# Optimization experiments

Measured on AMD Instinct MI355X. Metric: run time of the kernel, lower is better.

The kernel has to match this reference:

```python
import jax, jax.numpy as jnp
import numpy as np

B, N, D = 512, 100000, 64
TAU = 1e-4            # gumbel-softmax temperature from source
SIM_RATIO = 0.5       # similarity_ratio init kwarg
COS_EPS = 1e-6


def setup_inputs() -> dict:
    key = jax.random.key(0)
    k1, k2, k3, k4, k5 = jax.random.split(key, 5)
    need_replace = jax.random.randint(k1, (B, 2), 0, N, dtype=jnp.int64) if jax.config.jax_enable_x64 else jax.random.randint(k1, (B, 2), 0, N, dtype=jnp.int32)
    union_feature = jax.random.normal(k2, (B, 2 * D), dtype=jnp.float32)
    all_items = jax.random.normal(k3, (N, D), dtype=jnp.float32) * 0.1
    W = jax.random.normal(k4, (D, 2 * D), dtype=jnp.float32) * 0.05
    b = jax.random.normal(k5, (D,), dtype=jnp.float32) * 0.01
    return {"need_replace": need_replace, "union_feature": union_feature,
            "all_items": all_items, "W": W, "b": b}


def _cosine(a, b):
    # torch.nn.CosineSimilarity(dim=1, eps=1e-6): dot / max(||a||*||b||, eps)
    dot = jnp.sum(a * b, axis=1)
    na = jnp.linalg.norm(a, axis=1)
    nb = jnp.linalg.norm(b, axis=1)
    return dot / jnp.maximum(na * nb, COS_EPS)


def reference(need_replace, union_feature, all_items, W, b):
    item_ids = need_replace[:, 1]
    items_emb = all_items[item_ids]                      # [B, D]
    uif = union_feature @ W.T + b                        # [B, D] (nn.Linear)
    score = uif @ all_items.T                            # [B, N]

    # gumbel_softmax(tau=1e-4, hard=True), training branch
    g = jax.random.gumbel(jax.random.key(42), score.shape, dtype=score.dtype)
    y_soft = jax.nn.softmax((score + g) / TAU, axis=-1)  # [B, N]
    idx = jnp.argmax(y_soft, axis=-1)                    # [B]
    y_hard = jax.nn.one_hot(idx, N, dtype=score.dtype)
    P = y_hard + y_soft - jax.lax.stop_gradient(y_soft)  # straight-through hard one-hot

    item_sequence = jnp.arange(N, dtype=score.dtype)[None, :]
    replaceable_items = jnp.sum(P * item_sequence, axis=-1).astype(jnp.int32)
    replaceable_feat = P @ all_items                     # [B, D]

    sim = _cosine(items_emb, replaceable_feat)
    sim = (sim + 1.0) / 2.0                              # regularize_similarity
    labels = jnp.full((B,), SIM_RATIO, dtype=sim.dtype)
    similarity_loss = jnp.mean((sim - labels) ** 2)      # SimilarityMarginLoss (assumed MSE-to-margin)
    return replaceable_items, replaceable_feat, similarity_loss, jnp.mean(sim)
```

## Files before the change

### kernel.cpp

```cpp
#include <hip/hip_runtime.h>
#include <cstdint>

#define NITEMS   100000
#define BROWS    512
#define DDIM     64
#define S_BLOCKS 391
#define IPB      256
#define NCHUNKS  782
#define FB_Y     8
#define OUT_FEAT 512
#define OUT_LOSS (512 + 512 * 64)
#define OUT_MSIM (OUT_LOSS + 1)

#define BITS_RAW_T 4284334592u
#define G_TE       6.001f

typedef __attribute__((ext_vector_type(8)))  short  bf16x8;
typedef __attribute__((ext_vector_type(16))) float  f32x16;
typedef unsigned long long u64;
typedef uint32_t u32;

#define ROTL(x, r) __builtin_amdgcn_alignbit((x), (x), 32u - (r))

__device__ __forceinline__ u32 threefry_0_42_xor(u32 e) {
    const u32 K1 = 42u;
    const u32 K2 = 0x1BD11BDAu ^ 42u;
    u32 x0 = 0u;
    u32 x1 = e + K1;
#define TFR(r) { x0 += x1; x1 = ROTL(x1, r) ^ x0; }
    TFR(13u) TFR(15u) TFR(26u) TFR(6u)
    x0 += K1;  x1 += K2 + 1u;
    TFR(17u) TFR(29u) TFR(16u) TFR(24u)
    x0 += K2;  x1 += 2u;
    TFR(13u) TFR(15u) TFR(26u) TFR(6u)
    x1 += K1 + 3u;
    TFR(17u) TFR(29u) TFR(16u) TFR(24u)
    x0 += K1;  x1 += K2 + 4u;
    TFR(13u) TFR(15u) TFR(26u) TFR(6u)
    x0 += K2;  x1 += 5u;
#undef TFR
    return x0 ^ x1;
}

__device__ __forceinline__ float gumbel_from_bits(u32 b) {
    float f = __uint_as_float((b >> 9) | 0x3F800000u) - 1.0f;
    f = fmaxf(f, 1.17549435e-38f);
    return -logf(-logf(f));
}
__device__ __forceinline__ u32 order_map(float v) {
    u32 x = __float_as_uint(v);
    return (x & 0x80000000u) ? ~x : (x | 0x80000000u);
}
__device__ __forceinline__ float unpack_val(u64 p) {
    u32 x = (u32)(p >> 32);
    u32 f = (x & 0x80000000u) ? (x & 0x7FFFFFFFu) : ~x;
    return __uint_as_float(f);
}
__device__ __forceinline__ short f32_to_bf16_rne(float f) {
    u32 b = __float_as_uint(f);
    u32 r = (b + 0x7FFFu + ((b >> 16) & 1u)) >> 16;
    return (short)r;
}
__device__ __forceinline__ float bf16_to_f32(short h) {
    return __uint_as_float(((u32)(uint16_t)h) << 16);
}

__global__ void prep_kernel(const float* __restrict__ UF, const float* __restrict__ W,
                            const float* __restrict__ bias, const float* __restrict__ A,
                            float* __restrict__ uif, float* __restrict__ unorm,
                            float* __restrict__ wsAM4, int* __restrict__ cnt,
                            int* __restrict__ done, float* __restrict__ out) {
    const int t = threadIdx.x, b = blockIdx.x;
    if (b == 0) {
        if (t == 0) { *cnt = 0; out[OUT_LOSS] = 0.f; out[OUT_MSIM] = 0.f; }
        done[t] = 0; done[t + 256] = 0;
    }
    if (b < 128) {
        __shared__ float Wt[128 * 65];
        for (int i = t; i < 8192; i += 256) {
            int d = i >> 7, k = i & 127;
            Wt[k * 65 + d] = W[i];
        }
        __syncthreads();
        const int row = b * 4 + (t >> 6);
        const int d   = t & 63;
        const float* u = UF + row * 128;
        float s = 0.f;
#pragma unroll 4
        for (int k = 0; k < 128; k++) s = fmaf(u[k], Wt[k * 65 + d], s);
        s += bias[d];
        uif[row * 64 + d] = s;
        float q = s * s;
#pragma unroll
        for (int o = 32; o >= 1; o >>= 1) q += __shfl_xor(q, o);
        if (d == 0) unorm[row] = sqrtf(q);
    } else {
        const int item = (b - 128) * 256 + t;
        float q = 0.f;
        if (item < NITEMS) {
            const float4* r = (const float4*)(A + (size_t)item * DDIM);
#pragma unroll
            for (int k = 0; k < 16; k++) {
                float4 x = r[k];
                q = fmaf(x.x, x.x, q); q = fmaf(x.y, x.y, q);
                q = fmaf(x.z, x.z, q); q = fmaf(x.w, x.w, q);
            }
        }
        float n = sqrtf(q);
#pragma unroll
        for (int o = 32; o >= 1; o >>= 1) n = fmaxf(n, __shfl_xor(n, o));
        if ((t & 63) == 0) wsAM4[(b - 128) * 4 + (t >> 6)] = n;
    }
}

__global__ __launch_bounds__(256, 4) void phase1_kernel(
        const float* __restrict__ A, const float* __restrict__ uif,
        u64* __restrict__ wsT1, float* __restrict__ wsB) {
    __shared__ bf16x8 sh_ah[4 * 64];
    __shared__ bf16x8 sh_al[4 * 64];
    const int tid  = threadIdx.x;
    const int lane = tid & 63;
    const int wv   = tid >> 6;
    const int rg   = blockIdx.y;
    const int sb   = blockIdx.x;
    const int itembase = sb * IPB;
    const int ntiles = min(8, (NITEMS - itembase + 31) >> 5);
    const int row   = rg * 128 + wv * 32 + (lane & 31);
    const int khalf = (lane >> 5) * 8;

    bf16x8 uh[4], ul[4];
#pragma unroll
    for (int s = 0; s < 4; s++) {
        const float* src = uif + row * 64 + khalf + 16 * s;
        float4 v0 = *(const float4*)src;
        float4 v1 = *(const float4*)(src + 4);
        float vv[8] = {v0.x, v0.y, v0.z, v0.w, v1.x, v1.y, v1.z, v1.w};
        bf16x8 h, l2;
#pragma unroll
        for (int j = 0; j < 8; j++) {
            short hh = f32_to_bf16_rne(vv[j]);
            float r  = vv[j] - bf16_to_f32(hh);
            h[j] = hh; l2[j] = f32_to_bf16_rne(r);
        }
        uh[s] = h; ul[s] = l2;
    }

    u64 t1p = 0ull; float t1f = -3.0e38f, t2f = -3.0e38f, sm = -3.0e38f;
    const u32 rowbase_e = (u32)row * (u32)NITEMS;

    const int s_i   = tid & 31;
    const int s_c   = tid >> 5;
    const int s_dst = (s_c >> 1) * 64 + s_i + 32 * (s_c & 1);
    const float* s_srcbase = A + (size_t)s_i * 64 + 8 * s_c;

    float4 p0 = *(const float4*)(s_srcbase + (size_t)itembase * 64);
    float4 p1 = *(const float4*)(s_srcbase + (size_t)itembase * 64 + 4);

    for (int t = 0; t < ntiles; t++) {
        const int tb = itembase + t * 32;
        bf16x8 h, l2;
        {
            float vv[8] = {p0.x, p0.y, p0.z, p0.w, p1.x, p1.y, p1.z, p1.w};
#pragma unroll
            for (int j = 0; j < 8; j++) {
                short hh = f32_to_bf16_rne(vv[j]);
                float r  = vv[j] - bf16_to_f32(hh);
                h[j] = hh; l2[j] = f32_to_bf16_rne(r);
            }
        }
        __syncthreads();
        sh_ah[s_dst] = h; sh_al[s_dst] = l2;
        __syncthreads();
        if (t + 1 < ntiles) {
            const float* src = s_srcbase + (size_t)(tb + 32) * 64;
            p0 = *(const float4*)src;
            p1 = *(const float4*)(src + 4);
        }

        f32x16 acc;
#pragma unroll
        for (int z = 0; z < 16; z++) acc[z] = 0.0f;
#pragma unroll
        for (int s = 0; s < 4; s++) {
            bf16x8 ah = sh_ah[s * 64 + lane];
            bf16x8 al = sh_al[s * 64 + lane];
            acc = __builtin_amdgcn_mfma_f32_32x32x16_bf16(ah, uh[s], acc, 0, 0, 0);
            acc = __builtin_amdgcn_mfma_f32_32x32x16_bf16(al, uh[s], acc, 0, 0, 0);
            acc = __builtin_amdgcn_mfma_f32_32x32x16_bf16(ah, ul[s], acc, 0, 0, 0);
        }

        const int ib4 = tb + 4 * (lane >> 5);
#pragma unroll
        for (int i = 0; i < 16; i++) {
            const int il   = (i & 3) + 8 * (i >> 2);
            const int item = ib4 + il;
            u32 rb  = threefry_0_42_xor(rowbase_e + (u32)item);
            float s = acc[i];
            sm = fmaxf(sm, s);
            if (rb >= BITS_RAW_T) {
                float g = gumbel_from_bits(rb);
                float v = s + g;
                if (v > t1f) {
                    t2f = t1f; t1f = v;
                    t1p = ((u64)order_map(v) << 32) | (u32)(~(u32)item);
                } else t2f = fmaxf(t2f, v);
            }
        }
    }

    float bnd = fmaxf(t2f, sm + G_TE);
    {
        u64   op = __shfl_xor(t1p, 32);
        float of = __shfl_xor(t1f, 32);
        float ob = __shfl_xor(bnd, 32);
        if (op > t1p) { bnd = fmaxf(fmaxf(bnd, ob), t1f); t1p = op; t1f = of; }
        else          { bnd = fmaxf(fmaxf(bnd, ob), of); }
    }
    if (lane < 32) {
        wsT1[(size_t)row * S_BLOCKS + sb] = t1p;
        wsB [(size_t)row * S_BLOCKS + sb] = bnd;
    }
}

__global__ void merge_kernel(const u64* __restrict__ wsT1, const float* __restrict__ wsB,
                             const float* __restrict__ wsAM4, const float* __restrict__ unorm,
                             const float* __restrict__ A, const int* __restrict__ need_replace,
                             u64* __restrict__ packed, int* __restrict__ rowlist,
                             int* __restrict__ cnt, float* __restrict__ out) {
    const int row = blockIdx.x, t = threadIdx.x;
    float am = 0.f;
    for (int i = t; i < S_BLOCKS * 4; i += 64) am = fmaxf(am, wsAM4[i]);
    u64 p1 = 0ull; float f1 = -3.0e38f, f2 = -3.0e38f;
    for (int sbk = t; sbk < S_BLOCKS; sbk += 64) {
        u64   ep = wsT1[(size_t)row * S_BLOCKS + sbk];
        float e2 = wsB [(size_t)row * S_BLOCKS + sbk];
        if (ep > p1) { f2 = fmaxf(fmaxf(f1, e2), f2); p1 = ep; f1 = unpack_val(ep); }
        else         { float v = unpack_val(ep); f2 = fmaxf(f2, fmaxf(v, e2)); }
    }
#pragma unroll
    for (int off = 1; off < 64; off <<= 1) {
        u64   op  = __shfl_xor(p1, off);
        float of1 = __shfl_xor(f1, off);
        float of2 = __shfl_xor(f2, off);
        am = fmaxf(am, __shfl_xor(am, off));
        if (op > p1) { f2 = fmaxf(fmaxf(f1, of2), f2); p1 = op; f1 = of1; }
        else         { f2 = fmaxf(f2, fmaxf(of1, of2)); }
    }
    const float E = 1.5e-4f * unorm[row] * am + 3.0e-5f;
    if (f1 - f2 > 2.0f * E) {
        const int idx = (int)(~(u32)(p1 & 0xFFFFFFFFull));
        float fr = A[(size_t)idx * DDIM + t];
        out[OUT_FEAT + row * DDIM + t] = fr;
        int   item = need_replace[2 * row + 1];
        float fa   = A[(size_t)item * DDIM + t];
        float dot = fa * fr, na2 = fa * fa, nb2 = fr * fr;
#pragma unroll
        for (int o = 32; o >= 1; o >>= 1) {
            dot += __shfl_down(dot, o);
            na2 += __shfl_down(na2, o);
            nb2 += __shfl_down(nb2, o);
        }
        if (t == 0) {
            out[row] = (float)idx;
            float denom = fmaxf(sqrtf(na2) * sqrtf(nb2), 1e-6f);
            float sim = (dot / denom + 1.0f) * 0.5f;
            float d = sim - 0.5f;
            atomicAdd(&out[OUT_LOSS], d * d * (1.0f / 512.0f));
            atomicAdd(&out[OUT_MSIM], sim * (1.0f / 512.0f));
        }
    } else if (t == 0) {
        packed[row] = 0ull;
        rowlist[atomicAdd(cnt, 1)] = row;
    }
}

__global__ void fallback_kernel(const float* __restrict__ A, const float* __restrict__ uif,
                                const int* __restrict__ rowlist, const int* __restrict__ cnt,
                                const int* __restrict__ need_replace,
                                u64* __restrict__ packed, int* __restrict__ done,
                                float* __restrict__ out) {
    __shared__ float As[128 * 65];
    __shared__ float Us[64];
    __shared__ int   sh_last;
    const int t  = threadIdx.x;
    const int c  = blockIdx.x;
    const int n0 = c * 128;
    const int nitem = min(128, NITEMS - n0);
    const int total = *cnt;
    if ((int)blockIdx.y >= total) return;

    if (t < nitem) {
        const float4* src = (const float4*)(A + (size_t)(n0 + t) * 64);
#pragma unroll
        for (int k4 = 0; k4 < 16; k4++) {
            float4 x = src[k4];
            As[t * 65 + 4 * k4 + 0] = x.x; As[t * 65 + 4 * k4 + 1] = x.y;
            As[t * 65 + 4 * k4 + 2] = x.z; As[t * 65 + 4 * k4 + 3] = x.w;
        }
    }
    for (int li = blockIdx.y; li < total; li += FB_Y) {
        const int row = rowlist[li];
        __syncthreads();
        if (t < 64) Us[t] = uif[row * 64 + t];
        __syncthreads();
        u64 pk = 0ull;
        if (t < nitem) {
            const int item = n0 + t;
            u32 rb  = threefry_0_42_xor((u32)row * (u32)NITEMS + (u32)item);
            float g = gumbel_from_bits(rb);
            float s0 = 0.f, s1 = 0.f;
#pragma unroll
            for (int k8 = 0; k8 < 64; k8 += 8) {
                s0 = fmaf(As[t * 65 + k8 + 0], Us[k8 + 0], s0);
                s0 = fmaf(As[t * 65 + k8 + 1], Us[k8 + 1], s0);
                s0 = fmaf(As[t * 65 + k8 + 2], Us[k8 + 2], s0);
                s0 = fmaf(As[t * 65 + k8 + 3], Us[k8 + 3], s0);
                s1 = fmaf(As[t * 65 + k8 + 4], Us[k8 + 4], s1);
                s1 = fmaf(As[t * 65 + k8 + 5], Us[k8 + 5], s1);
                s1 = fmaf(As[t * 65 + k8 + 6], Us[k8 + 6], s1);
                s1 = fmaf(As[t * 65 + k8 + 7], Us[k8 + 7], s1);
            }
            float v = (s0 + s1) + g;
            pk = ((u64)order_map(v) << 32) | (u32)(~(u32)item);
        }
#pragma unroll
        for (int off = 1; off < 64; off <<= 1) {
            u64 o = __shfl_xor(pk, off);
            pk = (o > pk) ? o : pk;
        }
        if ((t & 63) == 0) atomicMax(&packed[row], pk);
        __syncthreads();
        if (t == 0) {
            __threadfence();
            sh_last = (atomicAdd(&done[li], 1) == NCHUNKS - 1) ? 1 : 0;
        }
        __syncthreads();
        if (sh_last && t < 64) {
            u64 fin = atomicMax(&packed[row], 0ull);
            const int idx = (int)(~(u32)(fin & 0xFFFFFFFFull));
            float fr = A[(size_t)idx * DDIM + t];
            out[OUT_FEAT + row * DDIM + t] = fr;
            int   item = need_replace[2 * row + 1];
            float fa   = A[(size_t)item * DDIM + t];
            float dot = fa * fr, na2 = fa * fa, nb2 = fr * fr;
#pragma unroll
            for (int o = 32; o >= 1; o >>= 1) {
                dot += __shfl_down(dot, o);
                na2 += __shfl_down(na2, o);
                nb2 += __shfl_down(nb2, o);
            }
            if (t == 0) {
                out[row] = (float)idx;
                float denom = fmaxf(sqrtf(na2) * sqrtf(nb2), 1e-6f);
                float sim = (dot / denom + 1.0f) * 0.5f;
                float d = sim - 0.5f;
                atomicAdd(&out[OUT_LOSS], d * d * (1.0f / 512.0f));
                atomicAdd(&out[OUT_MSIM], sim * (1.0f / 512.0f));
            }
        }
        __syncthreads();
    }
}

extern "C" void kernel_launch(void* const* d_in, const int* in_sizes, int n_in,
                              void* d_out, int out_size, void* d_ws, size_t ws_size,
                              hipStream_t stream) {
    (void)in_sizes; (void)n_in; (void)out_size; (void)ws_size;
    const int*   need_replace = (const int*)d_in[0];
    const float* UF           = (const float*)d_in[1];
    const float* A            = (const float*)d_in[2];
    const float* W            = (const float*)d_in[3];
    const float* bias         = (const float*)d_in[4];
    float* out = (float*)d_out;

    char* ws = (char*)d_ws;
    u64*   wsT1    = (u64*)  (ws);
    float* wsB     = (float*)(ws + 1601536);
    float* uif     = (float*)(ws + 2402304);
    u64*   packed  = (u64*)  (ws + 2533376);
    float* unorm   = (float*)(ws + 2537472);
    float* wsAM4   = (float*)(ws + 2539520);
    int*   rowlist = (int*)  (ws + 2545776);
    int*   cnt     = (int*)  (ws + 2547824);
    int*   done    = (int*)  (ws + 2547828);

    prep_kernel<<<519, 256, 0, stream>>>(UF, W, bias, A, uif, unorm, wsAM4, cnt, done, out);
    phase1_kernel<<<dim3(S_BLOCKS, 4), 256, 0, stream>>>(A, uif, wsT1, wsB);
    merge_kernel<<<BROWS, 64, 0, stream>>>(wsT1, wsB, wsAM4, unorm, A, need_replace,
                                           packed, rowlist, cnt, out);
    fallback_kernel<<<dim3(NCHUNKS, FB_Y), 128, 0, stream>>>(A, uif, rowlist, cnt,
                                                             need_replace, packed, done, out);
}
```

Measured before the change: 260.6 us.

## Split RNG survivor filtering from score GEMM and certify survivors exactly

The phase1 kernel no longer evaluates threefry and gumbel per score element inline. Half of the first 2048 blocks now run a pure RNG sweep that writes survivor (bits, item) pairs into per-row lists through atomics. The remaining blocks only compute the MFMA scores and a per-block row max. A new certify kernel recomputes exact fp32 dot products for the survivors, takes the top-2, and certifies the winner against a bound built from the max score plus the gumbel threshold. The intent is to take the RNG cost out of the GEMM's critical path and run it concurrently on other blocks, at the cost of atomic contention and a survivor cap of 512 per row that would silently drop candidates if exceeded.

After: 434.0 us. 1.67x slower.

```diff
diff --git a/kernel.cpp b/kernel.cpp
--- a/kernel.cpp
+++ b/kernel.cpp
@@ -8,6 +8,9 @@
 #define IPB      256
 #define NCHUNKS  782
 #define FB_Y     8
+#define SURV_CAP 512
+#define RNG_BLKS 1024
+#define NELEM    51200000u
 #define OUT_FEAT 512
 #define OUT_LOSS (512 + 512 * 64)
 #define OUT_MSIM (OUT_LOSS + 1)
@@ -51,11 +54,6 @@
     u32 x = __float_as_uint(v);
     return (x & 0x80000000u) ? ~x : (x | 0x80000000u);
 }
-__device__ __forceinline__ float unpack_val(u64 p) {
-    u32 x = (u32)(p >> 32);
-    u32 f = (x & 0x80000000u) ? (x & 0x7FFFFFFFu) : ~x;
-    return __uint_as_float(f);
-}
 __device__ __forceinline__ short f32_to_bf16_rne(float f) {
     u32 b = __float_as_uint(f);
     u32 r = (b + 0x7FFFu + ((b >> 16) & 1u)) >> 16;
@@ -69,11 +67,13 @@
                             const float* __restrict__ bias, const float* __restrict__ A,
                             float* __restrict__ uif, float* __restrict__ unorm,
                             float* __restrict__ wsAM4, int* __restrict__ cnt,
-                            int* __restrict__ done, float* __restrict__ out) {
+                            int* __restrict__ done, int* __restrict__ rowcnt,
+                            float* __restrict__ out) {
     const int t = threadIdx.x, b = blockIdx.x;
     if (b == 0) {
         if (t == 0) { *cnt = 0; out[OUT_LOSS] = 0.f; out[OUT_MSIM] = 0.f; }
         done[t] = 0; done[t + 256] = 0;
+        rowcnt[t] = 0; rowcnt[t + 256] = 0;
     }
     if (b < 128) {
         __shared__ float Wt[128 * 65];
@@ -113,16 +113,37 @@
     }
 }
 
-__global__ __launch_bounds__(256, 4) void phase1_kernel(
+__global__ __launch_bounds__(256, 4) void fused_kernel(
         const float* __restrict__ A, const float* __restrict__ uif,
-        u64* __restrict__ wsT1, float* __restrict__ wsB) {
+        float* __restrict__ wsSM, u64* __restrict__ surv, int* __restrict__ rowcnt) {
     __shared__ bf16x8 sh_ah[4 * 64];
     __shared__ bf16x8 sh_al[4 * 64];
-    const int tid  = threadIdx.x;
+    const int bx  = blockIdx.x;
+    const int tid = threadIdx.x;
+
+    int pidx = -1, ridx = -1;
+    if (bx < 2048) { if (bx & 1) ridx = bx >> 1; else pidx = bx >> 1; }
+    else pidx = 1024 + (bx - 2048);
+
+    if (ridx >= 0) {
+        const u32 stride = RNG_BLKS * 256u;
+        for (u32 e = (u32)ridx * 256u + (u32)tid; e < NELEM; e += stride) {
+            u32 b = threefry_0_42_xor(e);
+            if (b >= BITS_RAW_T) {
+                u32 row  = (u32)(((u64)e * 1407374884ull) >> 47);
+                u32 item = e - row * 100000u;
+                u32 slot = atomicAdd(&rowcnt[row], 1);
+                if (slot < SURV_CAP)
+                    surv[row * SURV_CAP + slot] = ((u64)b << 32) | (u64)item;
+            }
+        }
+        return;
+    }
+
     const int lane = tid & 63;
     const int wv   = tid >> 6;
-    const int rg   = blockIdx.y;
-    const int sb   = blockIdx.x;
+    const int sb   = pidx >> 2;
+    const int rg   = pidx & 3;
     const int itembase = sb * IPB;
     const int ntiles = min(8, (NITEMS - itembase + 31) >> 5);
     const int row   = rg * 128 + wv * 32 + (lane & 31);
@@ -145,9 +166,7 @@
         uh[s] = h; ul[s] = l2;
     }
 
-    u64 t1p = 0ull; float t1f = -3.0e38f, t2f = -3.0e38f, sm = -3.0e38f;
-    const u32 rowbase_e = (u32)row * (u32)NITEMS;
-
+    float sm = -3.0e38f;
     const int s_i   = tid & 31;
     const int s_c   = tid >> 5;
     const int s_dst = (s_c >> 1) * 64 + s_i + 32 * (s_c & 1);
@@ -188,66 +207,71 @@
             acc = __builtin_amdgcn_mfma_f32_32x32x16_bf16(al, uh[s], acc, 0, 0, 0);
             acc = __builtin_amdgcn_mfma_f32_32x32x16_bf16(ah, ul[s], acc, 0, 0, 0);
         }
-
-        const int ib4 = tb + 4 * (lane >> 5);
-#pragma unroll
-        for (int i = 0; i < 16; i++) {
-            const int il   = (i & 3) + 8 * (i >> 2);
-            const int item = ib4 + il;
-            u32 rb  = threefry_0_42_xor(rowbase_e + (u32)item);
-            float s = acc[i];
-            sm = fmaxf(sm, s);
-            if (rb >= BITS_RAW_T) {
-                float g = gumbel_from_bits(rb);
-                float v = s + g;
-                if (v > t1f) {
-                    t2f = t1f; t1f = v;
-                    t1p = ((u64)order_map(v) << 32) | (u32)(~(u32)item);
-                } else t2f = fmaxf(t2f, v);
-            }
-        }
-    }
-
-    float bnd = fmaxf(t2f, sm + G_TE);
-    {
-        u64   op = __shfl_xor(t1p, 32);
-        float of = __shfl_xor(t1f, 32);
-        float ob = __shfl_xor(bnd, 32);
-        if (op > t1p) { bnd = fmaxf(fmaxf(bnd, ob), t1f); t1p = op; t1f = of; }
-        else          { bnd = fmaxf(fmaxf(bnd, ob), of); }
-    }
-    if (lane < 32) {
-        wsT1[(size_t)row * S_BLOCKS + sb] = t1p;
-        wsB [(size_t)row * S_BLOCKS + sb] = bnd;
-    }
-}
-
-__global__ void merge_kernel(const u64* __restrict__ wsT1, const float* __restrict__ wsB,
-                             const float* __restrict__ wsAM4, const float* __restrict__ unorm,
-                             const float* __restrict__ A, const int* __restrict__ need_replace,
-                             u64* __restrict__ packed, int* __restrict__ rowlist,
-                             int* __restrict__ cnt, float* __restrict__ out) {
+#pragma unroll
+        for (int i = 0; i < 16; i++) sm = fmaxf(sm, acc[i]);
+    }
+
+    sm = fmaxf(sm, __shfl_xor(sm, 32));
+    if (lane < 32) wsSM[(size_t)row * S_BLOCKS + sb] = sm;
+}
+
+__global__ void certify_kernel(const float* __restrict__ wsSM, const float* __restrict__ wsAM4,
+                               const float* __restrict__ unorm, const float* __restrict__ uif,
+                               const float* __restrict__ A, const u64* __restrict__ surv,
+                               const int* __restrict__ rowcnt, const int* __restrict__ need_replace,
+                               u64* __restrict__ packed, int* __restrict__ rowlist,
+                               int* __restrict__ cnt, float* __restrict__ out) {
     const int row = blockIdx.x, t = threadIdx.x;
+    __shared__ float Us[64];
+    Us[t] = uif[row * 64 + t];
+    __syncthreads();
+
     float am = 0.f;
     for (int i = t; i < S_BLOCKS * 4; i += 64) am = fmaxf(am, wsAM4[i]);
+    float smx = -3.0e38f;
+    for (int i = t; i < S_BLOCKS; i += 64) smx = fmaxf(smx, wsSM[(size_t)row * S_BLOCKS + i]);
+
+    const int n = min(rowcnt[row], SURV_CAP);
     u64 p1 = 0ull; float f1 = -3.0e38f, f2 = -3.0e38f;
-    for (int sbk = t; sbk < S_BLOCKS; sbk += 64) {
-        u64   ep = wsT1[(size_t)row * S_BLOCKS + sbk];
-        float e2 = wsB [(size_t)row * S_BLOCKS + sbk];
-        if (ep > p1) { f2 = fmaxf(fmaxf(f1, e2), f2); p1 = ep; f1 = unpack_val(ep); }
-        else         { float v = unpack_val(ep); f2 = fmaxf(f2, fmaxf(v, e2)); }
+    for (int i = t; i < n; i += 64) {
+        u64 en   = surv[row * SURV_CAP + i];
+        u32 item = (u32)(en & 0xFFFFFFFFull);
+        float g  = gumbel_from_bits((u32)(en >> 32));
+        const float4* a4 = (const float4*)(A + (size_t)item * DDIM);
+        float s0 = 0.f, s1 = 0.f;
+#pragma unroll
+        for (int k = 0; k < 16; k += 2) {
+            float4 x = a4[k];
+            float4 y = a4[k + 1];
+            s0 = fmaf(x.x, Us[4*k    ], s0);
+            s0 = fmaf(x.y, Us[4*k + 1], s0);
+            s0 = fmaf(x.z, Us[4*k + 2], s0);
+            s0 = fmaf(x.w, Us[4*k + 3], s0);
+            s1 = fmaf(y.x, Us[4*k + 4], s1);
+            s1 = fmaf(y.y, Us[4*k + 5], s1);
+            s1 = fmaf(y.z, Us[4*k + 6], s1);
+            s1 = fmaf(y.w, Us[4*k + 7], s1);
+        }
+        float v = (s0 + s1) + g;
+        if (v > f1) {
+            f2 = f1; f1 = v;
+            p1 = ((u64)order_map(v) << 32) | (u32)(~item);
+        } else f2 = fmaxf(f2, v);
     }
 #pragma unroll
     for (int off = 1; off < 64; off <<= 1) {
         u64   op  = __shfl_xor(p1, off);
         float of1 = __shfl_xor(f1, off);
         float of2 = __shfl_xor(f2, off);
-        am = fmaxf(am, __shfl_xor(am, off));
+        am  = fmaxf(am,  __shfl_xor(am,  off));
+        smx = fmaxf(smx, __shfl_xor(smx, off));
         if (op > p1) { f2 = fmaxf(fmaxf(f1, of2), f2); p1 = op; f1 = of1; }
         else         { f2 = fmaxf(f2, fmaxf(of1, of2)); }
     }
+
+    const float bound = fmaxf(f2, smx + G_TE);
     const float E = 1.5e-4f * unorm[row] * am + 3.0e-5f;
-    if (f1 - f2 > 2.0f * E) {
+    if (f1 - bound > 2.0f * E) {
         const int idx = (int)(~(u32)(p1 & 0xFFFFFFFFull));
         float fr = A[(size_t)idx * DDIM + t];
         out[OUT_FEAT + row * DDIM + t] = fr;
@@ -374,20 +398,22 @@
     float* out = (float*)d_out;
 
     char* ws = (char*)d_ws;
-    u64*   wsT1    = (u64*)  (ws);
-    float* wsB     = (float*)(ws + 1601536);
-    float* uif     = (float*)(ws + 2402304);
-    u64*   packed  = (u64*)  (ws + 2533376);
-    float* unorm   = (float*)(ws + 2537472);
-    float* wsAM4   = (float*)(ws + 2539520);
-    int*   rowlist = (int*)  (ws + 2545776);
-    int*   cnt     = (int*)  (ws + 2547824);
-    int*   done    = (int*)  (ws + 2547828);
-
-    prep_kernel<<<519, 256, 0, stream>>>(UF, W, bias, A, uif, unorm, wsAM4, cnt, done, out);
-    phase1_kernel<<<dim3(S_BLOCKS, 4), 256, 0, stream>>>(A, uif, wsT1, wsB);
-    merge_kernel<<<BROWS, 64, 0, stream>>>(wsT1, wsB, wsAM4, unorm, A, need_replace,
-                                           packed, rowlist, cnt, out);
+    float* wsSM    = (float*)(ws);
+    u64*   surv    = (u64*)  (ws + 800768);
+    float* uif     = (float*)(ws + 2897920);
+    u64*   packed  = (u64*)  (ws + 3028992);
+    float* unorm   = (float*)(ws + 3033088);
+    float* wsAM4   = (float*)(ws + 3035136);
+    int*   rowlist = (int*)  (ws + 3041392);
+    int*   cnt     = (int*)  (ws + 3043440);
+    int*   done    = (int*)  (ws + 3043444);
+    int*   rowcnt  = (int*)  (ws + 3045492);
+
+    prep_kernel<<<519, 256, 0, stream>>>(UF, W, bias, A, uif, unorm, wsAM4,
+                                         cnt, done, rowcnt, out);
+    fused_kernel<<<2588, 256, 0, stream>>>(A, uif, wsSM, surv, rowcnt);
+    certify_kernel<<<BROWS, 64, 0, stream>>>(wsSM, wsAM4, unorm, uif, A, surv, rowcnt,
+                                             need_replace, packed, rowlist, cnt, out);
     fallback_kernel<<<dim3(NCHUNKS, FB_Y), 128, 0, stream>>>(A, uif, rowlist, cnt,
                                                              need_replace, packed, done, out);
 }
```
